# Performance work log

Measured on AMD Instinct MI355X. Metric: run time of the kernel, lower is better.

Reference implementation:

```python
import jax, jax.numpy as jnp
import numpy as np

N_EMBD = 1024
N_HEADS = 16
HEAD_SIZE = N_EMBD // N_HEADS
BLOCK_SIZE = 2048
BATCH = 2
SEQ = 2048
EPS = 1e-5


def setup_inputs() -> dict:
    key = jax.random.key(0)
    ks = jax.random.split(key, 12)
    s = 0.02
    x = jax.random.normal(ks[0], (BATCH, SEQ, N_EMBD), dtype=jnp.float32)
    # per-head Q/K/V weights concatenated: [n_embd, n_heads*head_size]
    Wq = jax.random.normal(ks[1], (N_EMBD, N_EMBD), dtype=jnp.float32) * s
    Wk = jax.random.normal(ks[2], (N_EMBD, N_EMBD), dtype=jnp.float32) * s
    Wv = jax.random.normal(ks[3], (N_EMBD, N_EMBD), dtype=jnp.float32) * s
    Wproj = jax.random.normal(ks[4], (N_EMBD, N_EMBD), dtype=jnp.float32) * s
    bproj = jnp.zeros((N_EMBD,), dtype=jnp.float32)
    W1 = jax.random.normal(ks[5], (N_EMBD, 4 * N_EMBD), dtype=jnp.float32) * s
    b1 = jnp.zeros((4 * N_EMBD,), dtype=jnp.float32)
    W2 = jax.random.normal(ks[6], (4 * N_EMBD, N_EMBD), dtype=jnp.float32) * s
    b2 = jnp.zeros((N_EMBD,), dtype=jnp.float32)
    ln1_w = jnp.ones((N_EMBD,), dtype=jnp.float32)
    ln1_b = jnp.zeros((N_EMBD,), dtype=jnp.float32)
    ln2_w = jnp.ones((N_EMBD,), dtype=jnp.float32)
    ln2_b = jnp.zeros((N_EMBD,), dtype=jnp.float32)
    return dict(x=x, Wq=Wq, Wk=Wk, Wv=Wv, Wproj=Wproj, bproj=bproj,
                W1=W1, b1=b1, W2=W2, b2=b2,
                ln1_w=ln1_w, ln1_b=ln1_b, ln2_w=ln2_w, ln2_b=ln2_b)


def _layer_norm(x, w, b):
    mu = jnp.mean(x, axis=-1, keepdims=True)
    var = jnp.var(x, axis=-1, keepdims=True)
    return (x - mu) * jax.lax.rsqrt(var + EPS) * w + b


def reference(x, Wq, Wk, Wv, Wproj, bproj, W1, b1, W2, b2, ln1_w, ln1_b, ln2_w, ln2_b):
    B, T, C = x.shape
    # --- attention sub-block (pre-LN) ---
    h = _layer_norm(x, ln1_w, ln1_b)
    # project then split heads: [B,T,H,D] -> [B,H,T,D]
    def split(W):
        return (h @ W).reshape(B, T, N_HEADS, HEAD_SIZE).transpose(0, 2, 1, 3)
    q, k, v = split(Wq), split(Wk), split(Wv)
    # NOTE: original code scales by C**-0.5 with C = n_embd (not head_size)
    scores = jnp.einsum('bhtd,bhsd->bhts', q, k) * (C ** -0.5)  # [B,H,T,T]
    causal = jnp.tril(jnp.ones((T, T), dtype=bool))
    scores = jnp.where(causal, scores, -jnp.inf)
    wei = jax.nn.softmax(scores, axis=-1)
    attn = jnp.einsum('bhts,bhsd->bhtd', wei, v)  # [B,H,T,D]
    attn = attn.transpose(0, 2, 1, 3).reshape(B, T, C)  # concat heads
    x = x + attn @ Wproj + bproj
    # --- FFN sub-block (pre-LN) ---
    h2 = _layer_norm(x, ln2_w, ln2_b)
    ff = jax.nn.relu(h2 @ W1 + b1) @ W2 + b2
    return x + ff
```

## Files before the change

kernel.cpp:

```cpp
#include <hip/hip_runtime.h>
#include <cstdint>

typedef __attribute__((ext_vector_type(8))) __bf16 bf16_8;
typedef __attribute__((ext_vector_type(4))) __bf16 bf16_4;
typedef __attribute__((ext_vector_type(4))) float f32x4;

#define QSCALE 0.045084220027780106f

__device__ __forceinline__ void gld_lds16(const __bf16* g, __bf16* l) {
  __builtin_amdgcn_global_load_lds(
      (const __attribute__((address_space(1))) void*)(void*)g,
      (__attribute__((address_space(3))) void*)l, 16, 0, 0);
}

__global__ __launch_bounds__(256) void convt_k(
    const float* __restrict__ Wq, const float* __restrict__ Wk,
    const float* __restrict__ Wv, const float* __restrict__ Wp,
    const float* __restrict__ W1, const float* __restrict__ W2,
    __bf16* __restrict__ WqT, __bf16* __restrict__ WkT,
    __bf16* __restrict__ WvT, __bf16* __restrict__ WpT,
    __bf16* __restrict__ W1T, __bf16* __restrict__ W2T) {
  int bid = blockIdx.x;
  const float* in; __bf16* outp; int Kd, Nd, tile;
  if (bid < 4096) {
    int m = bid >> 10; tile = bid & 1023; Kd = 1024; Nd = 1024;
    in   = m == 0 ? Wq  : m == 1 ? Wk  : m == 2 ? Wv  : Wp;
    outp = m == 0 ? WqT : m == 1 ? WkT : m == 2 ? WvT : WpT;
  } else if (bid < 8192) {
    tile = bid - 4096; Kd = 1024; Nd = 4096; in = W1; outp = W1T;
  } else {
    tile = bid - 8192; Kd = 4096; Nd = 1024; in = W2; outp = W2T;
  }
  int tilesN = Nd >> 5;
  int tk = tile / tilesN, tn = tile % tilesN;
  int k0 = tk * 32, n0 = tn * 32;
  __shared__ float tbuf[32][33];
  int tx = threadIdx.x & 31, ty = threadIdx.x >> 5;
#pragma unroll
  for (int i = 0; i < 4; ++i)
    tbuf[ty + i * 8][tx] = in[(size_t)(k0 + ty + i * 8) * Nd + (n0 + tx)];
  __syncthreads();
#pragma unroll
  for (int i = 0; i < 4; ++i)
    outp[(size_t)(n0 + ty + i * 8) * Kd + (k0 + tx)] = (__bf16)tbuf[tx][ty + i * 8];
}

__global__ __launch_bounds__(256) void ln_k(const float* __restrict__ x,
                                            const float* __restrict__ w,
                                            const float* __restrict__ b,
                                            __bf16* __restrict__ out) {
  int row = blockIdx.x;
  int tid = threadIdx.x;
  f32x4 v = *(const f32x4*)(x + (size_t)row * 1024 + tid * 4);
  float s = v[0] + v[1] + v[2] + v[3];
  float sq = v[0] * v[0] + v[1] * v[1] + v[2] * v[2] + v[3] * v[3];
#pragma unroll
  for (int m = 1; m < 64; m <<= 1) { s += __shfl_xor(s, m); sq += __shfl_xor(sq, m); }
  __shared__ float rs[4], rq[4];
  int wave = tid >> 6, lane = tid & 63;
  if (lane == 0) { rs[wave] = s; rq[wave] = sq; }
  __syncthreads();
  s  = rs[0] + rs[1] + rs[2] + rs[3];
  sq = rq[0] + rq[1] + rq[2] + rq[3];
  float mu   = s * (1.f / 1024.f);
  float var  = sq * (1.f / 1024.f) - mu * mu;
  float rstd = rsqrtf(var + 1e-5f);
  f32x4 wv = *(const f32x4*)(w + tid * 4);
  f32x4 bv = *(const f32x4*)(b + tid * 4);
  bf16_4 o;
#pragma unroll
  for (int i = 0; i < 4; ++i) o[i] = (__bf16)((v[i] - mu) * rstd * wv[i] + bv[i]);
  *(bf16_4*)(out + (size_t)row * 1024 + tid * 4) = o;
}

template <int MODE, int BM, int BN, int BK>
__global__ __launch_bounds__(256) void gemm_k(
    const __bf16* __restrict__ A,
    const __bf16* __restrict__ B0, const __bf16* __restrict__ B1,
    const __bf16* __restrict__ B2,
    __bf16* __restrict__ O0, __bf16* __restrict__ O1, __bf16* __restrict__ O2,
    float* __restrict__ Of,
    const float* __restrict__ bias, const float* __restrict__ res,
    int K, int Nchunk, int nBlkM, int nBlkN) {
  constexpr int NC = BK / 8;
  constexpr int MT = BM / 32, NT = BN / 32;
  constexpr int KK = BK / 32;
  constexpr int RPC = 64 / NC;
  constexpr int CA = BM / RPC / 4;
  constexpr int CB = BN / RPC / 4;
  __shared__ __align__(16) __bf16 As[2][BM * BK];
  __shared__ __align__(16) __bf16 Bs[2][BN * BK];
  int chunk = blockIdx.y;
  const __bf16* Bt = chunk == 0 ? B0 : (chunk == 1 ? B1 : B2);
  __bf16* Ob       = chunk == 0 ? O0 : (chunk == 1 ? O1 : O2);
  int pid = blockIdx.x;
  const int GM = 8;
  int perG = GM * nBlkN;
  int gid = pid / perG;
  int fm = gid * GM;
  int gsz = min(nBlkM - fm, GM);
  int bm = fm + (pid % gsz);
  int bn = (pid % perG) / gsz;
  int m0 = bm * BM, n0 = bn * BN;
  int tid = threadIdx.x, wave = tid >> 6, lane = tid & 63;
  int quad = lane >> 4, l16 = lane & 15;
  int wm = (wave & 1) * (BM / 2), wn = (wave >> 1) * (BN / 2);
  int srow = lane / NC, schunk = lane % NC;

  f32x4 z = {0.f, 0.f, 0.f, 0.f};
  f32x4 acc[MT][NT];
#pragma unroll
  for (int mt = 0; mt < MT; ++mt)
#pragma unroll
    for (int nt = 0; nt < NT; ++nt) acc[mt][nt] = z;

  const __bf16* Ag = A  + (size_t)m0 * K;
  const __bf16* Bg = Bt + (size_t)n0 * K;

  auto stage = [&](int k0, int buf) {
#pragma unroll
    for (int i = 0; i < CA; ++i) {
      int r0 = (wave * CA + i) * RPC;
      int gc = schunk ^ ((r0 + srow) & (NC - 1));
      gld_lds16(Ag + (size_t)(r0 + srow) * K + k0 + gc * 8, &As[buf][r0 * BK]);
    }
#pragma unroll
    for (int i = 0; i < CB; ++i) {
      int r0 = (wave * CB + i) * RPC;
      int gc = schunk ^ ((r0 + srow) & (NC - 1));
      gld_lds16(Bg + (size_t)(r0 + srow) * K + k0 + gc * 8, &Bs[buf][r0 * BK]);
    }
  };

  auto compute = [&](int buf) {
#pragma unroll
    for (int kk = 0; kk < KK; ++kk) {
      bf16_8 af[MT], bfr[NT];
#pragma unroll
      for (int t = 0; t < MT; ++t) {
        int r = wm + t * 16 + l16;
        int lc = (kk * 4 + quad) ^ (r & (NC - 1));
        af[t] = *(const bf16_8*)(&As[buf][r * BK + lc * 8]);
      }
#pragma unroll
      for (int t = 0; t < NT; ++t) {
        int r = wn + t * 16 + l16;
        int lc = (kk * 4 + quad) ^ (r & (NC - 1));
        bfr[t] = *(const bf16_8*)(&Bs[buf][r * BK + lc * 8]);
      }
#pragma unroll
      for (int mt = 0; mt < MT; ++mt)
#pragma unroll
        for (int nt = 0; nt < NT; ++nt)
          acc[mt][nt] = __builtin_amdgcn_mfma_f32_16x16x32_bf16(af[mt], bfr[nt],
                                                                acc[mt][nt], 0, 0, 0);
    }
  };

  int niter = K / BK;
  stage(0, 0);
  __syncthreads();
  for (int it = 0; it < niter - 1; ++it) {
    stage((it + 1) * BK, (it + 1) & 1);
    compute(it & 1);
    __syncthreads();
  }
  compute((niter - 1) & 1);

  if (MODE == 0 && chunk == 2) {
#pragma unroll
    for (int mt = 0; mt < MT; ++mt) {
      int mbase = m0 + wm + mt * 16 + quad * 4;
      int bb = mbase >> 11, tt = mbase & 2047;
#pragma unroll
      for (int nt = 0; nt < NT; ++nt) {
        int n = n0 + wn + nt * 16 + l16;
        bf16_4 pk;
#pragma unroll
        for (int r = 0; r < 4; ++r) pk[r] = (__bf16)acc[mt][nt][r];
        *(bf16_4*)(O2 + ((size_t)((bb * 16 + (n >> 6)) * 64 + (n & 63))) * 2048 + tt) = pk;
      }
    }
    return;
  }

  float oscale = (MODE == 0 && chunk == 0) ? QSCALE : 1.0f;
#pragma unroll
  for (int mt = 0; mt < MT; ++mt) {
#pragma unroll
    for (int r = 0; r < 4; ++r) {
      int m = m0 + wm + mt * 16 + quad * 4 + r;
      size_t rowo = (size_t)m * Nchunk;
#pragma unroll
      for (int nt = 0; nt < NT; ++nt) {
        int n = n0 + wn + nt * 16 + l16;
        float v = acc[mt][nt][r];
        if (MODE == 0) {
          Ob[rowo + n] = (__bf16)(v * oscale);
        } else if (MODE == 1) {
          v += bias[n]; v = v > 0.f ? v : 0.f;
          Ob[rowo + n] = (__bf16)v;
        } else {
          v += bias[n] + res[rowo + n];
          Of[rowo + n] = v;
        }
      }
    }
  }
}

__global__ __launch_bounds__(256) void attn_k(const __bf16* __restrict__ Q,
                                              const __bf16* __restrict__ K,
                                              const __bf16* __restrict__ Vt,
                                              __bf16* __restrict__ O) {
  __shared__ __align__(16) __bf16 Kls[2][64 * 64];
  __shared__ __align__(16) __bf16 Vls[2][64 * 64];
  __shared__ __align__(16) __bf16 Pls[4][32 * 72];

  int i = blockIdx.x;
  int qt, bh;
  if (i < 256) { qt = 15 - (i >> 5); bh = i & 31; }
  else         { qt = (i - 256) >> 5; bh = i & 31; }
  int h = bh & 15, b = bh >> 4;
  int q0 = qt * 128;
  int tid = threadIdx.x, wave = tid >> 6, lane = tid & 63;
  int quad = lane >> 4, l16 = lane & 15;
  int qw = q0 + wave * 32;
  int r8 = lane >> 3, c8 = lane & 7;
  int cswz = c8 ^ r8;
  int so0 = (quad ^ (l16 & 7)) * 8;
  int so1 = so0 ^ 32;

  bf16_8 qf[2][2];
#pragma unroll
  for (int g = 0; g < 2; ++g) {
    const __bf16* Qg = Q + ((size_t)(b * 2048 + qw + g * 16 + l16)) * 1024 + h * 64;
    qf[g][0] = *(const bf16_8*)(Qg + quad * 8);
    qf[g][1] = *(const bf16_8*)(Qg + 32 + quad * 8);
  }

  const __bf16* Kb = K + (size_t)(b * 2048) * 1024 + h * 64;
  const __bf16* Vh = Vt + (size_t)((b * 16 + h) * 64) * 2048;

  f32x4 z = {0.f, 0.f, 0.f, 0.f};
  f32x4 ot[2][4];
#pragma unroll
  for (int g = 0; g < 2; ++g)
#pragma unroll
    for (int dt = 0; dt < 4; ++dt) ot[g][dt] = z;
  float l_acc[2] = {0.f, 0.f};
  __bf16* Pw = &Pls[wave][0];

  auto stage = [&](int kt, int buf) {
#pragma unroll
    for (int i2 = 0; i2 < 2; ++i2) {
      int rl = wave * 16 + i2 * 8 + r8;
      gld_lds16(Kb + (size_t)(kt + rl) * 1024 + cswz * 8,
                &Kls[buf][(wave * 16 + i2 * 8) * 64]);
      gld_lds16(Vh + (size_t)rl * 2048 + kt + cswz * 8,
                &Vls[buf][(wave * 16 + i2 * 8) * 64]);
    }
  };

  int ntiles = 2 * (qt + 1);
  stage(0, 0);
  __syncthreads();
  for (int it = 0; it < ntiles; ++it) {
    int kt = it * 64;
    int buf = it & 1;
    if (it + 1 < ntiles) stage((it + 1) * 64, buf ^ 1);
    if (kt <= qw + 31) {
      bool masked = (kt + 63 > qw);
      f32x4 sf[2][4];
#pragma unroll
      for (int kk = 0; kk < 4; ++kk) {
        const __bf16* kr = &Kls[buf][(kk * 16 + l16) * 64];
        bf16_8 ka = *(const bf16_8*)(kr + so0);
        bf16_8 kb = *(const bf16_8*)(kr + so1);
#pragma unroll
        for (int g = 0; g < 2; ++g) {
          f32x4 a = z;
          a = __builtin_amdgcn_mfma_f32_16x16x32_bf16(ka, qf[g][0], a, 0, 0, 0);
          a = __builtin_amdgcn_mfma_f32_16x16x32_bf16(kb, qf[g][1], a, 0, 0, 0);
          sf[g][kk] = a;
        }
      }
#pragma unroll
      for (int g = 0; g < 2; ++g) {
        int qrow = qw + g * 16 + l16;
#pragma unroll
        for (int kk = 0; kk < 4; ++kk) {
          bf16_4 pk;
#pragma unroll
          for (int r = 0; r < 4; ++r) {
            float x = sf[g][kk][r];
            if (masked && (kt + kk * 16 + quad * 4 + r > qrow)) x = -1e30f;
            float p = __builtin_amdgcn_exp2f(x);
            l_acc[g] += p;
            pk[r] = (__bf16)p;
          }
          *(bf16_4*)(Pw + (g * 16 + l16) * 72 + kk * 16 + quad * 4) = pk;
        }
      }
      bf16_8 pf[2][2];
#pragma unroll
      for (int g = 0; g < 2; ++g) {
        pf[g][0] = *(const bf16_8*)(Pw + (g * 16 + l16) * 72 + quad * 8);
        pf[g][1] = *(const bf16_8*)(Pw + (g * 16 + l16) * 72 + 32 + quad * 8);
      }
#pragma unroll
      for (int dt = 0; dt < 4; ++dt) {
        const __bf16* vr = &Vls[buf][(dt * 16 + l16) * 64];
        bf16_8 v0 = *(const bf16_8*)(vr + so0);
        bf16_8 v1 = *(const bf16_8*)(vr + so1);
#pragma unroll
        for (int g = 0; g < 2; ++g) {
          ot[g][dt] = __builtin_amdgcn_mfma_f32_16x16x32_bf16(v0, pf[g][0], ot[g][dt], 0, 0, 0);
          ot[g][dt] = __builtin_amdgcn_mfma_f32_16x16x32_bf16(v1, pf[g][1], ot[g][dt], 0, 0, 0);
        }
      }
    }
    __syncthreads();
  }

#pragma unroll
  for (int g = 0; g < 2; ++g) {
    float l = l_acc[g];
    l += __shfl_xor(l, 16);
    l += __shfl_xor(l, 32);
    float inv = 1.0f / l;
    size_t base = (size_t)(b * 2048 + qw + g * 16 + l16) * 1024 + h * 64;
#pragma unroll
    for (int dt = 0; dt < 4; ++dt) {
      bf16_4 ok;
#pragma unroll
      for (int r = 0; r < 4; ++r) ok[r] = (__bf16)(ot[g][dt][r] * inv);
      *(bf16_4*)(O + base + dt * 16 + quad * 4) = ok;
    }
  }
}

extern "C" void kernel_launch(void* const* d_in, const int* in_sizes, int n_in,
                              void* d_out, int out_size, void* d_ws,
                              size_t ws_size, hipStream_t stream) {
  const float* x   = (const float*)d_in[0];
  const float* Wq  = (const float*)d_in[1];
  const float* Wk  = (const float*)d_in[2];
  const float* Wv  = (const float*)d_in[3];
  const float* Wp  = (const float*)d_in[4];
  const float* bp  = (const float*)d_in[5];
  const float* W1  = (const float*)d_in[6];
  const float* b1  = (const float*)d_in[7];
  const float* W2  = (const float*)d_in[8];
  const float* b2  = (const float*)d_in[9];
  const float* l1w = (const float*)d_in[10];
  const float* l1b = (const float*)d_in[11];
  const float* l2w = (const float*)d_in[12];
  const float* l2b = (const float*)d_in[13];
  float* out = (float*)d_out;
  char* ws = (char*)d_ws;
  const size_t MB = 1024ull * 1024ull;
  __bf16* WqT = (__bf16*)(ws + 0 * MB);
  __bf16* WkT = (__bf16*)(ws + 2 * MB);
  __bf16* WvT = (__bf16*)(ws + 4 * MB);
  __bf16* WpT = (__bf16*)(ws + 6 * MB);
  __bf16* W1T = (__bf16*)(ws + 8 * MB);
  __bf16* W2T = (__bf16*)(ws + 16 * MB);
  __bf16* hb  = (__bf16*)(ws + 24 * MB);
  __bf16* Qb  = (__bf16*)(ws + 32 * MB);
  __bf16* Kb_ = (__bf16*)(ws + 40 * MB);
  __bf16* Vt  = (__bf16*)(ws + 48 * MB);
  __bf16* Ab  = (__bf16*)(ws + 56 * MB);
  __bf16* F1  = (__bf16*)(ws + 64 * MB);

  convt_k<<<12288, 256, 0, stream>>>(Wq, Wk, Wv, Wp, W1, W2,
                                     WqT, WkT, WvT, WpT, W1T, W2T);
  ln_k<<<4096, 256, 0, stream>>>(x, l1w, l1b, hb);
  gemm_k<0, 128, 128, 32><<<dim3(256, 3), 256, 0, stream>>>(
      hb, WqT, WkT, WvT, Qb, Kb_, Vt, nullptr, nullptr, nullptr,
      1024, 1024, 32, 8);
  attn_k<<<512, 256, 0, stream>>>(Qb, Kb_, Vt, Ab);
  gemm_k<2, 64, 64, 64><<<dim3(1024, 1), 256, 0, stream>>>(
      Ab, WpT, WpT, WpT, nullptr, nullptr, nullptr, out, bp, x,
      1024, 1024, 64, 16);
  ln_k<<<4096, 256, 0, stream>>>(out, l2w, l2b, hb);
  gemm_k<1, 128, 128, 32><<<dim3(1024, 1), 256, 0, stream>>>(
      hb, W1T, W1T, W1T, F1, F1, F1, nullptr, b1, nullptr,
      1024, 4096, 32, 32);
  gemm_k<2, 64, 64, 64><<<dim3(1024, 1), 256, 0, stream>>>(
      F1, W2T, W2T, W2T, nullptr, nullptr, nullptr, out, b2, out,
      4096, 1024, 64, 16);
}
```

Before: 348.4 us.

## Rebalance causal attention with paired query groups and split-KV wave roles

```diff
diff --git a/kernel.cpp b/kernel.cpp
--- a/kernel.cpp
+++ b/kernel.cpp
@@ -213,75 +213,76 @@
                                               const __bf16* __restrict__ K,
                                               const __bf16* __restrict__ Vt,
                                               __bf16* __restrict__ O) {
-  __shared__ __align__(16) __bf16 Kls[2][64 * 64];
-  __shared__ __align__(16) __bf16 Vls[2][64 * 64];
   __shared__ __align__(16) __bf16 Pls[4][32 * 72];
+  __shared__ __align__(16) float Obuf[2][32][68];
+  __shared__ float Lbuf[2][32][4];
 
   int i = blockIdx.x;
-  int qt, bh;
-  if (i < 256) { qt = 15 - (i >> 5); bh = i & 31; }
-  else         { qt = (i - 256) >> 5; bh = i & 31; }
+  int bh = i & 31, p = i >> 5;
   int h = bh & 15, b = bh >> 4;
-  int q0 = qt * 128;
   int tid = threadIdx.x, wave = tid >> 6, lane = tid & 63;
   int quad = lane >> 4, l16 = lane & 15;
-  int qw = q0 + wave * 32;
-  int r8 = lane >> 3, c8 = lane & 7;
-  int cswz = c8 ^ r8;
-  int so0 = (quad ^ (l16 & 7)) * 8;
-  int so1 = so0 ^ 32;
-
-  bf16_8 qf[2][2];
-#pragma unroll
-  for (int g = 0; g < 2; ++g) {
-    const __bf16* Qg = Q + ((size_t)(b * 2048 + qw + g * 16 + l16)) * 1024 + h * 64;
-    qf[g][0] = *(const bf16_8*)(Qg + quad * 8);
-    qf[g][1] = *(const bf16_8*)(Qg + 32 + quad * 8);
-  }
+  int pr = wave >> 1;
+  int roleB = wave & 1;
+  int j = pr == 0 ? p : 31 - p;
+  int qg_lo = j, qg_hi = 63 - j;
+  int t_lo = (j >> 1) + 1;
+  int t_hi = 32 - (j >> 1);
+  int ksp = 17 - t_lo;
 
   const __bf16* Kb = K + (size_t)(b * 2048) * 1024 + h * 64;
   const __bf16* Vh = Vt + (size_t)((b * 16 + h) * 64) * 2048;
+  __bf16* Pw = &Pls[wave][0];
 
   f32x4 z = {0.f, 0.f, 0.f, 0.f};
+  bf16_8 qf[2][2];
   f32x4 ot[2][4];
-#pragma unroll
-  for (int g = 0; g < 2; ++g)
-#pragma unroll
-    for (int dt = 0; dt < 4; ++dt) ot[g][dt] = z;
-  float l_acc[2] = {0.f, 0.f};
-  __bf16* Pw = &Pls[wave][0];
-
-  auto stage = [&](int kt, int buf) {
-#pragma unroll
-    for (int i2 = 0; i2 < 2; ++i2) {
-      int rl = wave * 16 + i2 * 8 + r8;
-      gld_lds16(Kb + (size_t)(kt + rl) * 1024 + cswz * 8,
-                &Kls[buf][(wave * 16 + i2 * 8) * 64]);
-      gld_lds16(Vh + (size_t)rl * 2048 + kt + cswz * 8,
-                &Vls[buf][(wave * 16 + i2 * 8) * 64]);
-    }
-  };
-
-  int ntiles = 2 * (qt + 1);
-  stage(0, 0);
-  __syncthreads();
-  for (int it = 0; it < ntiles; ++it) {
-    int kt = it * 64;
-    int buf = it & 1;
-    if (it + 1 < ntiles) stage((it + 1) * 64, buf ^ 1);
-    if (kt <= qw + 31) {
+  float l_acc[2];
+
+  auto loadQ = [&](int qg) {
+#pragma unroll
+    for (int g = 0; g < 2; ++g) {
+      const __bf16* Qg = Q + ((size_t)(b * 2048 + qg * 32 + g * 16 + l16)) * 1024 + h * 64;
+      qf[g][0] = *(const bf16_8*)(Qg + quad * 8);
+      qf[g][1] = *(const bf16_8*)(Qg + 32 + quad * 8);
+    }
+  };
+
+  auto zacc = [&]() {
+#pragma unroll
+    for (int g = 0; g < 2; ++g) {
+#pragma unroll
+      for (int dt = 0; dt < 4; ++dt) ot[g][dt] = z;
+      l_acc[g] = 0.f;
+    }
+  };
+
+  auto process = [&](int qg, int it0, int it1) {
+    int qw = qg * 32;
+    for (int it = it0; it < it1; ++it) {
+      int kt = it * 64;
       bool masked = (kt + 63 > qw);
+      bf16_8 kfr[4][2], vfr[4][2];
+#pragma unroll
+      for (int kk = 0; kk < 4; ++kk) {
+        const __bf16* kr = Kb + (size_t)(kt + kk * 16 + l16) * 1024 + quad * 8;
+        kfr[kk][0] = *(const bf16_8*)(kr);
+        kfr[kk][1] = *(const bf16_8*)(kr + 32);
+      }
+#pragma unroll
+      for (int dt = 0; dt < 4; ++dt) {
+        const __bf16* vr = Vh + (size_t)(dt * 16 + l16) * 2048 + kt + quad * 8;
+        vfr[dt][0] = *(const bf16_8*)(vr);
+        vfr[dt][1] = *(const bf16_8*)(vr + 32);
+      }
       f32x4 sf[2][4];
 #pragma unroll
       for (int kk = 0; kk < 4; ++kk) {
-        const __bf16* kr = &Kls[buf][(kk * 16 + l16) * 64];
-        bf16_8 ka = *(const bf16_8*)(kr + so0);
-        bf16_8 kb = *(const bf16_8*)(kr + so1);
 #pragma unroll
         for (int g = 0; g < 2; ++g) {
           f32x4 a = z;
-          a = __builtin_amdgcn_mfma_f32_16x16x32_bf16(ka, qf[g][0], a, 0, 0, 0);
-          a = __builtin_amdgcn_mfma_f32_16x16x32_bf16(kb, qf[g][1], a, 0, 0, 0);
+          a = __builtin_amdgcn_mfma_f32_16x16x32_bf16(kfr[kk][0], qf[g][0], a, 0, 0, 0);
+          a = __builtin_amdgcn_mfma_f32_16x16x32_bf16(kfr[kk][1], qf[g][1], a, 0, 0, 0);
           sf[g][kk] = a;
         }
       }
@@ -295,9 +296,9 @@
           for (int r = 0; r < 4; ++r) {
             float x = sf[g][kk][r];
             if (masked && (kt + kk * 16 + quad * 4 + r > qrow)) x = -1e30f;
-            float p = __builtin_amdgcn_exp2f(x);
-            l_acc[g] += p;
-            pk[r] = (__bf16)p;
+            float pp = __builtin_amdgcn_exp2f(x);
+            l_acc[g] += pp;
+            pk[r] = (__bf16)pp;
           }
           *(bf16_4*)(Pw + (g * 16 + l16) * 72 + kk * 16 + quad * 4) = pk;
         }
@@ -310,33 +311,62 @@
       }
 #pragma unroll
       for (int dt = 0; dt < 4; ++dt) {
-        const __bf16* vr = &Vls[buf][(dt * 16 + l16) * 64];
-        bf16_8 v0 = *(const bf16_8*)(vr + so0);
-        bf16_8 v1 = *(const bf16_8*)(vr + so1);
 #pragma unroll
         for (int g = 0; g < 2; ++g) {
-          ot[g][dt] = __builtin_amdgcn_mfma_f32_16x16x32_bf16(v0, pf[g][0], ot[g][dt], 0, 0, 0);
-          ot[g][dt] = __builtin_amdgcn_mfma_f32_16x16x32_bf16(v1, pf[g][1], ot[g][dt], 0, 0, 0);
+          ot[g][dt] = __builtin_amdgcn_mfma_f32_16x16x32_bf16(vfr[dt][0], pf[g][0], ot[g][dt], 0, 0, 0);
+          ot[g][dt] = __builtin_amdgcn_mfma_f32_16x16x32_bf16(vfr[dt][1], pf[g][1], ot[g][dt], 0, 0, 0);
         }
       }
     }
-    __syncthreads();
-  }
-
-#pragma unroll
-  for (int g = 0; g < 2; ++g) {
-    float l = l_acc[g];
-    l += __shfl_xor(l, 16);
-    l += __shfl_xor(l, 32);
-    float inv = 1.0f / l;
-    size_t base = (size_t)(b * 2048 + qw + g * 16 + l16) * 1024 + h * 64;
-#pragma unroll
-    for (int dt = 0; dt < 4; ++dt) {
-      bf16_4 ok;
-#pragma unroll
-      for (int r = 0; r < 4; ++r) ok[r] = (__bf16)(ot[g][dt][r] * inv);
-      *(bf16_4*)(O + base + dt * 16 + quad * 4) = ok;
-    }
+  };
+
+  auto writeO = [&](int qg, const float* lc) {
+#pragma unroll
+    for (int g = 0; g < 2; ++g) {
+      float l = lc[g];
+      l += __shfl_xor(l, 16);
+      l += __shfl_xor(l, 32);
+      float inv = 1.0f / l;
+      size_t base = (size_t)(b * 2048 + qg * 32 + g * 16 + l16) * 1024 + h * 64;
+#pragma unroll
+      for (int dt = 0; dt < 4; ++dt) {
+        bf16_4 ok;
+#pragma unroll
+        for (int r = 0; r < 4; ++r) ok[r] = (__bf16)(ot[g][dt][r] * inv);
+        *(bf16_4*)(O + base + dt * 16 + quad * 4) = ok;
+      }
+    }
+  };
+
+  if (roleB) {
+    loadQ(qg_hi); zacc();
+    process(qg_hi, ksp, t_hi);
+#pragma unroll
+    for (int g = 0; g < 2; ++g) {
+#pragma unroll
+      for (int dt = 0; dt < 4; ++dt)
+        *(f32x4*)&Obuf[pr][g * 16 + l16][dt * 16 + quad * 4] = ot[g][dt];
+      Lbuf[pr][g * 16 + l16][quad] = l_acc[g];
+    }
+  } else {
+    loadQ(qg_lo); zacc();
+    process(qg_lo, 0, t_lo);
+    writeO(qg_lo, l_acc);
+    loadQ(qg_hi); zacc();
+    process(qg_hi, 0, ksp);
+  }
+  __syncthreads();
+  if (!roleB) {
+#pragma unroll
+    for (int g = 0; g < 2; ++g) {
+#pragma unroll
+      for (int dt = 0; dt < 4; ++dt)
+        ot[g][dt] += *(const f32x4*)&Obuf[pr][g * 16 + l16][dt * 16 + quad * 4];
+    }
+    float lc[2];
+#pragma unroll
+    for (int g = 0; g < 2; ++g) lc[g] = l_acc[g] + Lbuf[pr][g * 16 + l16][quad];
+    writeO(qg_hi, lc);
   }
 }
 
```

Measured after the change: 351.6 us. No clear change (+0.9%).

## Pair complementary causal query tiles in one 512-thread attention block sharing K/V

Applied to the files above, without the earlier changes.

```diff
diff --git a/kernel.cpp b/kernel.cpp
--- a/kernel.cpp
+++ b/kernel.cpp
@@ -209,66 +209,58 @@
   }
 }
 
-__global__ __launch_bounds__(256) void attn_k(const __bf16* __restrict__ Q,
+__global__ __launch_bounds__(512) void attn_k(const __bf16* __restrict__ Q,
                                               const __bf16* __restrict__ K,
                                               const __bf16* __restrict__ Vt,
                                               __bf16* __restrict__ O) {
   __shared__ __align__(16) __bf16 Kls[2][64 * 64];
   __shared__ __align__(16) __bf16 Vls[2][64 * 64];
-  __shared__ __align__(16) __bf16 Pls[4][32 * 72];
+  __shared__ __align__(16) __bf16 Pls[8][32 * 72];
 
   int i = blockIdx.x;
-  int qt, bh;
-  if (i < 256) { qt = 15 - (i >> 5); bh = i & 31; }
-  else         { qt = (i - 256) >> 5; bh = i & 31; }
+  int bh = i & 31, j = i >> 5;
   int h = bh & 15, b = bh >> 4;
-  int q0 = qt * 128;
+  int qtA = 15 - j, qtB = j;
+  int nT = 2 * (qtA + 1);
   int tid = threadIdx.x, wave = tid >> 6, lane = tid & 63;
   int quad = lane >> 4, l16 = lane & 15;
-  int qw = q0 + wave * 32;
   int r8 = lane >> 3, c8 = lane & 7;
   int cswz = c8 ^ r8;
   int so0 = (quad ^ (l16 & 7)) * 8;
   int so1 = so0 ^ 32;
-
+  int qt = wave < 4 ? qtA : qtB;
+  int qw = qt * 128 + (wave & 3) * 32;
+
+  const __bf16* Kb = K + (size_t)(b * 2048) * 1024 + h * 64;
+  const __bf16* Vh = Vt + (size_t)((b * 16 + h) * 64) * 2048;
+  __bf16* Pw = &Pls[wave][0];
+
+  f32x4 z = {0.f, 0.f, 0.f, 0.f};
   bf16_8 qf[2][2];
+  f32x4 ot[2][4];
+  float l_acc[2] = {0.f, 0.f};
+
 #pragma unroll
   for (int g = 0; g < 2; ++g) {
     const __bf16* Qg = Q + ((size_t)(b * 2048 + qw + g * 16 + l16)) * 1024 + h * 64;
     qf[g][0] = *(const bf16_8*)(Qg + quad * 8);
     qf[g][1] = *(const bf16_8*)(Qg + 32 + quad * 8);
-  }
-
-  const __bf16* Kb = K + (size_t)(b * 2048) * 1024 + h * 64;
-  const __bf16* Vh = Vt + (size_t)((b * 16 + h) * 64) * 2048;
-
-  f32x4 z = {0.f, 0.f, 0.f, 0.f};
-  f32x4 ot[2][4];
-#pragma unroll
-  for (int g = 0; g < 2; ++g)
 #pragma unroll
     for (int dt = 0; dt < 4; ++dt) ot[g][dt] = z;
-  float l_acc[2] = {0.f, 0.f};
-  __bf16* Pw = &Pls[wave][0];
+  }
 
   auto stage = [&](int kt, int buf) {
-#pragma unroll
-    for (int i2 = 0; i2 < 2; ++i2) {
-      int rl = wave * 16 + i2 * 8 + r8;
-      gld_lds16(Kb + (size_t)(kt + rl) * 1024 + cswz * 8,
-                &Kls[buf][(wave * 16 + i2 * 8) * 64]);
-      gld_lds16(Vh + (size_t)rl * 2048 + kt + cswz * 8,
-                &Vls[buf][(wave * 16 + i2 * 8) * 64]);
-    }
+    int rl = wave * 8 + r8;
+    gld_lds16(Kb + (size_t)(kt + rl) * 1024 + cswz * 8, &Kls[buf][(wave * 8) * 64]);
+    gld_lds16(Vh + (size_t)rl * 2048 + kt + cswz * 8, &Vls[buf][(wave * 8) * 64]);
   };
 
-  int ntiles = 2 * (qt + 1);
   stage(0, 0);
   __syncthreads();
-  for (int it = 0; it < ntiles; ++it) {
-    int kt = it * 64;
-    int buf = it & 1;
-    if (it + 1 < ntiles) stage((it + 1) * 64, buf ^ 1);
+  for (int t = 0; t < nT; ++t) {
+    int kt = t * 64;
+    int buf = t & 1;
+    if (t + 1 < nT) stage((t + 1) * 64, buf ^ 1);
     if (kt <= qw + 31) {
       bool masked = (kt + 63 > qw);
       f32x4 sf[2][4];
@@ -379,7 +371,7 @@
   gemm_k<0, 128, 128, 32><<<dim3(256, 3), 256, 0, stream>>>(
       hb, WqT, WkT, WvT, Qb, Kb_, Vt, nullptr, nullptr, nullptr,
       1024, 1024, 32, 8);
-  attn_k<<<512, 256, 0, stream>>>(Qb, Kb_, Vt, Ab);
+  attn_k<<<256, 512, 0, stream>>>(Qb, Kb_, Vt, Ab);
   gemm_k<2, 64, 64, 64><<<dim3(1024, 1), 256, 0, stream>>>(
       Ab, WpT, WpT, WpT, nullptr, nullptr, nullptr, out, bp, x,
       1024, 1024, 64, 16);
```

New measurement: 338.5 us. 2.8% less time.
